# Optimization experiments

Hardware: AMD Instinct MI355X
Metric: run time of the kernel (lower is better)

The kernel has to match this reference:

```python
import jax, jax.numpy as jnp
import numpy as np

D_MODEL, D_STATE, D_CONV, D_INNER, DT_RANK = 1024, 16, 4, 2048, 64
B_SZ, L = 4, 2048

def setup_inputs() -> dict:
    key = jax.random.key(0)
    ks = jax.random.split(key, 7)
    return {
        "hidden_states": jax.random.normal(ks[0], (B_SZ, L, D_MODEL), jnp.float32),
        "in_proj_w": jax.random.normal(ks[1], (2 * D_INNER, D_MODEL), jnp.float32) * (D_MODEL ** -0.5),
        "conv_w": jax.random.normal(ks[2], (D_INNER, 1, D_CONV), jnp.float32) * 0.5,
        "conv_b": jax.random.normal(ks[3], (D_INNER,), jnp.float32) * 0.1,
        "x_proj_w": jax.random.normal(ks[4], (DT_RANK + 2 * D_STATE, D_INNER), jnp.float32) * (D_INNER ** -0.5),
        "dt_proj_w": jax.random.normal(ks[5], (D_INNER, DT_RANK), jnp.float32) * (DT_RANK ** -0.5),
        "A_log": jax.random.uniform(ks[6], (D_INNER, D_STATE), jnp.float32, 0.0, 2.0),
    }

def reference(hidden_states, in_proj_w, conv_w, conv_b, x_proj_w, dt_proj_w, A_log):
    b, l, d = hidden_states.shape
    # in_proj: (b,l,d) x (2*d_inner,d)^T -> (b, 2*d_inner, l)
    xz = jnp.einsum('bld,ed->bel', hidden_states, in_proj_w)
    x, z = jnp.split(xz, 2, axis=1)  # each (b, d_inner, l); z unused downstream
    A = -jnp.exp(A_log)              # (d_inner, d_state)
    # causal depthwise conv1d (left pad d_conv-1) + SiLU
    x = jax.lax.conv_general_dilated(
        x, conv_w, window_strides=(1,), padding=[(D_CONV - 1, 0)],
        feature_group_count=D_INNER,
        dimension_numbers=('NCH', 'OIH', 'NCH'))
    x = jax.nn.silu(x + conv_b[None, :, None])  # (b, d_inner, l)
    # x_proj: (b,l,dt_rank+2*d_state)
    x_dbl = jnp.einsum('bdl,ed->ble', x, x_proj_w)
    dt, B_mat, C_mat = jnp.split(x_dbl, [DT_RANK, DT_RANK + D_STATE], axis=-1)
    dt = jnp.einsum('blr,dr->bdl', dt, dt_proj_w)          # (b, d_inner, l), no bias
    B_mat = jnp.swapaxes(B_mat, 1, 2)                      # (b, d_state, l)
    C_mat = jnp.swapaxes(C_mat, 1, 2)                      # (b, d_state, l)
    return (dt, A, B_mat, C_mat, x)
```

## Files before the change

### kernel.cpp

```cpp
#include <hip/hip_runtime.h>
#include <hip/hip_bf16.h>
#include <math.h>

#define D_MODEL 1024
#define D_STATE 16
#define D_CONV  4
#define D_INNER 2048
#define DT_RANK 64
#define B_SZ    4
#define L_SEQ   2048

#define OFF_DT 0
#define OFF_A  (B_SZ * D_INNER * L_SEQ)
#define OFF_B  (OFF_A + D_INNER * D_STATE)
#define OFF_C  (OFF_B + B_SZ * D_STATE * L_SEQ)
#define OFF_X  (OFF_C + B_SZ * D_STATE * L_SEQ)

typedef __attribute__((ext_vector_type(8))) short bf16x8;
typedef __attribute__((ext_vector_type(8))) unsigned short us8;
typedef __attribute__((ext_vector_type(4))) float f32x4;
typedef unsigned short ushort_t;
typedef unsigned int uint_t;

static __device__ __forceinline__ ushort_t f2bf(float f) {
  __hip_bfloat16 h = __float2bfloat16(f);
  return *(ushort_t*)&h;
}
static __device__ __forceinline__ float bf2f(ushort_t u) {
  union { uint_t u; float f; } c;
  c.u = ((uint_t)u) << 16;
  return c.f;
}

#define N4_HS   (B_SZ * L_SEQ * D_MODEL / 4)
#define N4_W    (D_INNER * D_MODEL / 4)
#define N4_XW   ((DT_RANK + 2 * D_STATE) * D_INNER / 4)
#define N4_DW   (D_INNER * DT_RANK / 4)
#define N4_Z0   (B_SZ * DT_RANK * L_SEQ / 4)
#define N4_Z1   (2 * B_SZ * D_STATE * L_SEQ / 4)
#define N4_A    (D_INNER * D_STATE / 4)
#define N4_TOT  (N4_HS + N4_W + N4_XW + N4_DW + N4_Z0 + N4_Z1 + N4_A)

__global__ __launch_bounds__(256) void k_prep(
    const float4* __restrict__ hs, const float4* __restrict__ ipw,
    const float4* __restrict__ xpw, const float4* __restrict__ dpw,
    const float4* __restrict__ alog,
    ushort4* __restrict__ bfHS, ushort4* __restrict__ bfW,
    ushort4* __restrict__ xwb, ushort4* __restrict__ dwb,
    float4* __restrict__ z0, float4* __restrict__ z1,
    float4* __restrict__ aout) {
  int i = blockIdx.x * 256 + threadIdx.x;
  if (i < N4_HS) {
    float4 v = hs[i];
    ushort4 o; o.x = f2bf(v.x); o.y = f2bf(v.y); o.z = f2bf(v.z); o.w = f2bf(v.w);
    bfHS[i] = o;
    return;
  }
  i -= N4_HS;
  if (i < N4_W) {
    float4 v = ipw[i];
    ushort4 o; o.x = f2bf(v.x); o.y = f2bf(v.y); o.z = f2bf(v.z); o.w = f2bf(v.w);
    bfW[i] = o;
    return;
  }
  i -= N4_W;
  if (i < N4_XW) {
    float4 v = xpw[i];
    ushort4 o; o.x = f2bf(v.x); o.y = f2bf(v.y); o.z = f2bf(v.z); o.w = f2bf(v.w);
    xwb[i] = o;
    return;
  }
  i -= N4_XW;
  if (i < N4_DW) {
    float4 v = dpw[i];
    ushort4 o; o.x = f2bf(v.x); o.y = f2bf(v.y); o.z = f2bf(v.z); o.w = f2bf(v.w);
    dwb[i] = o;
    return;
  }
  i -= N4_DW;
  if (i < N4_Z0) { z0[i] = (float4){0.f, 0.f, 0.f, 0.f}; return; }
  i -= N4_Z0;
  if (i < N4_Z1) { z1[i] = (float4){0.f, 0.f, 0.f, 0.f}; return; }
  i -= N4_Z1;
  if (i < N4_A) {
    float4 v = alog[i];
    float4 o;
    o.x = -expf(v.x); o.y = -expf(v.y); o.z = -expf(v.z); o.w = -expf(v.w);
    aout[i] = o;
  }
}

__global__ __launch_bounds__(256) void k_inproj_mfma(
    const ushort_t* __restrict__ Wb,
    const ushort_t* __restrict__ HSb,
    ushort_t* __restrict__ Cout) {
  const int flat = blockIdx.x + 16 * blockIdx.y + 256 * blockIdx.z;
  const int swz  = (flat & 7) * 128 + (flat >> 3);
  const int bn = swz & 15;
  const int bm = (swz >> 4) & 15;
  const int b  = swz >> 8;

  __shared__ ushort_t sh[128 * 136];
  const int tid  = threadIdx.x;
  const int wv   = tid >> 6;
  const int lane = tid & 63;
  const int wr = wv >> 1, wc = wv & 1;

  const int srow = tid >> 2;
  const int ss   = tid & 3;

  const ushort_t* Ag = Wb + (size_t)(bm * 128) * D_MODEL;
  const ushort_t* Bg = HSb + (size_t)b * L_SEQ * D_MODEL
                           + (size_t)(bn * 128) * D_MODEL;

  f32x4 acc[4][4];
#pragma unroll
  for (int i = 0; i < 4; ++i)
#pragma unroll
    for (int j = 0; j < 4; ++j) acc[i][j] = (f32x4){0.f, 0.f, 0.f, 0.f};

  const int ksel = lane >> 4;
  const int frow = lane & 15;

#define STAGE_IN(BUF, K0)                                                        \
  do {                                                                           \
    _Pragma("unroll")                                                            \
    for (int q = 0; q < 2; ++q) {                                                \
      int row = q * 64 + srow;                                                   \
      int xs  = ss ^ ((row >> 1) & 3);                                           \
      const ushort_t* ga = Ag + (size_t)row * D_MODEL + (K0) + xs * 8;           \
      const ushort_t* gb = Bg + (size_t)row * D_MODEL + (K0) + xs * 8;           \
      ushort_t* la = sh + (BUF) * 8192 + (q * 256 + wv * 64) * 8;                \
      ushort_t* lb = sh + (BUF) * 8192 + 4096 + (q * 256 + wv * 64) * 8;         \
      __builtin_amdgcn_global_load_lds((const __attribute__((address_space(1))) void*)ga, \
                                       (__attribute__((address_space(3))) void*)la, 16, 0, 0); \
      __builtin_amdgcn_global_load_lds((const __attribute__((address_space(1))) void*)gb, \
                                       (__attribute__((address_space(3))) void*)lb, 16, 0, 0); \
    }                                                                            \
  } while (0)

#define COMPUTE(BUF)                                                             \
  do {                                                                           \
    const ushort_t* Ab = sh + (BUF) * 8192;                                      \
    const ushort_t* Bb = sh + (BUF) * 8192 + 4096;                               \
    bf16x8 af[4], bfr[4];                                                        \
    _Pragma("unroll")                                                            \
    for (int m = 0; m < 4; ++m) {                                                \
      int row = wr * 64 + m * 16 + frow;                                         \
      af[m] = *(const bf16x8*)(Ab + (row * 4 + (ksel ^ ((row >> 1) & 3))) * 8);  \
    }                                                                            \
    _Pragma("unroll")                                                            \
    for (int n = 0; n < 4; ++n) {                                                \
      int row = wc * 64 + n * 16 + frow;                                         \
      bfr[n] = *(const bf16x8*)(Bb + (row * 4 + (ksel ^ ((row >> 1) & 3))) * 8); \
    }                                                                            \
    _Pragma("unroll")                                                            \
    for (int m = 0; m < 4; ++m)                                                  \
      _Pragma("unroll")                                                          \
      for (int n = 0; n < 4; ++n)                                                \
        acc[m][n] = __builtin_amdgcn_mfma_f32_16x16x32_bf16(af[m], bfr[n], acc[m][n], 0, 0, 0); \
  } while (0)

  STAGE_IN(0, 0);
  STAGE_IN(1, 32);
  asm volatile("s_waitcnt vmcnt(4)" ::: "memory");
  __builtin_amdgcn_s_barrier();

  for (int t = 0; t < 30; ++t) {
    COMPUTE(t & 1);
    __builtin_amdgcn_sched_barrier(0);
    __builtin_amdgcn_s_barrier();
    STAGE_IN(t & 1, (t + 2) * 32);
    asm volatile("s_waitcnt vmcnt(4)" ::: "memory");
    __builtin_amdgcn_s_barrier();
    __builtin_amdgcn_sched_barrier(0);
  }
  COMPUTE(0);
  __builtin_amdgcn_sched_barrier(0);
  __builtin_amdgcn_s_barrier();
  asm volatile("s_waitcnt vmcnt(0)" ::: "memory");
  __builtin_amdgcn_s_barrier();
  COMPUTE(1);
#undef STAGE_IN
#undef COMPUTE

  __syncthreads();

  const int crow0 = (lane >> 4) * 4;
  const int ccol  = lane & 15;
#pragma unroll
  for (int m = 0; m < 4; ++m) {
#pragma unroll
    for (int n = 0; n < 4; ++n) {
      int r0 = wr * 64 + m * 16 + crow0;
      int c  = wc * 64 + n * 16 + ccol;
#pragma unroll
      for (int i = 0; i < 4; ++i)
        sh[(r0 + i) * 136 + c] = f2bf(acc[m][n][i]);
    }
  }
  __syncthreads();
  ushort_t* Cb = Cout + (size_t)b * D_INNER * L_SEQ
                      + (size_t)(bm * 128) * L_SEQ + bn * 128;
#pragma unroll
  for (int q = 0; q < 8; ++q) {
    int idx = q * 256 + tid;
    int r   = idx >> 4;
    int c16 = idx & 15;
    us8 v = *(const us8*)(sh + r * 136 + c16 * 8);
    *(us8*)(Cb + (size_t)r * L_SEQ + c16 * 8) = v;
  }
}

__global__ __launch_bounds__(256) void k_xproj_fused(
    const ushort_t* __restrict__ XWb,
    const ushort_t* __restrict__ Xpre,
    const float* __restrict__ CW,
    const float* __restrict__ CB,
    float* __restrict__ Xout,
    float* __restrict__ XDBL,
    float* __restrict__ OutB,
    float* __restrict__ OutC) {
  const int ln = blockIdx.x;
  const int sk = blockIdx.y;
  const int b  = blockIdx.z;
  __shared__ ushort_t As[96 * 40];
  __shared__ ushort_t Bs[64 * 34];
  const int tid  = threadIdx.x;
  const int wv   = tid >> 6;
  const int lane = tid & 63;
  const int wr = wv >> 1, wc = wv & 1;
  const int ksel = lane >> 4;
  const int frow = lane & 15;

  f32x4 acc[3][2];
#pragma unroll
  for (int i = 0; i < 3; ++i)
#pragma unroll
    for (int j = 0; j < 2; ++j) acc[i][j] = (f32x4){0.f, 0.f, 0.f, 0.f};

  for (int k0 = 0; k0 < 512; k0 += 32) {
    const int koff = sk * 512 + k0;
    {
      int row = tid >> 2, s = tid & 3;
      bf16x8 v = *(const bf16x8*)(XWb + (size_t)row * D_INNER + koff + s * 8);
      *(bf16x8*)(As + row * 40 + s * 8) = v;
      if (tid < 128) {
        int row2 = 64 + (tid >> 2);
        bf16x8 v2 = *(const bf16x8*)(XWb + (size_t)row2 * D_INNER + koff + s * 8);
        *(bf16x8*)(As + row2 * 40 + s * 8) = v2;
      }
    }
    {
      int n4 = tid & 15;
      int kp = tid >> 4;
      int l0 = ln * 64 + 4 * n4;
      float sv[2][4];
#pragma unroll
      for (int r = 0; r < 2; ++r) {
        int d = koff + 2 * kp + r;
        const ushort_t* row = Xpre + ((size_t)b * D_INNER + d) * L_SEQ;
        ushort4 cur = *(const ushort4*)(row + l0);
        float em3 = 0.f, em2 = 0.f, em1 = 0.f;
        if (l0 >= 4) {
          ushort4 pv = *(const ushort4*)(row + l0 - 4);
          em3 = bf2f(pv.y); em2 = bf2f(pv.z); em1 = bf2f(pv.w);
        }
        float ee[7] = {em3, em2, em1, bf2f(cur.x), bf2f(cur.y), bf2f(cur.z), bf2f(cur.w)};
        float4 w = *(const float4*)(CW + d * 4);
        float bias = CB[d];
#pragma unroll
        for (int i = 0; i < 4; ++i) {
          float v = w.x * ee[i] + w.y * ee[i + 1] + w.z * ee[i + 2] + w.w * ee[i + 3] + bias;
          sv[r][i] = v / (1.f + expf(-v));
        }
        *(float4*)(Xout + ((size_t)b * D_INNER + d) * L_SEQ + l0) =
            make_float4(sv[r][0], sv[r][1], sv[r][2], sv[r][3]);
      }
#pragma unroll
      for (int i = 0; i < 4; ++i) {
        uint_t pk = (uint_t)f2bf(sv[0][i]) | ((uint_t)f2bf(sv[1][i]) << 16);
        *(uint_t*)(Bs + (4 * n4 + i) * 34 + 2 * kp) = pk;
      }
    }
    __syncthreads();

    bf16x8 af[3], bfr[2];
#pragma unroll
    for (int mi = 0; mi < 3; ++mi) {
      int row = wr * 48 + mi * 16 + frow;
      af[mi] = *(const bf16x8*)(As + row * 40 + ksel * 8);
    }
#pragma unroll
    for (int ni = 0; ni < 2; ++ni) {
      int n = wc * 32 + ni * 16 + frow;
      const uint_t* p = (const uint_t*)(Bs + n * 34);
      union { uint_t u[4]; bf16x8 v; } fr;
#pragma unroll
      for (int q = 0; q < 4; ++q) fr.u[q] = p[ksel * 4 + q];
      bfr[ni] = fr.v;
    }
#pragma unroll
    for (int mi = 0; mi < 3; ++mi)
#pragma unroll
      for (int ni = 0; ni < 2; ++ni)
        acc[mi][ni] = __builtin_amdgcn_mfma_f32_16x16x32_bf16(af[mi], bfr[ni], acc[mi][ni], 0, 0, 0);
    __syncthreads();
  }

  const int crow0 = (lane >> 4) * 4;
  const int ccol  = lane & 15;
#pragma unroll
  for (int mi = 0; mi < 3; ++mi) {
    int e0 = wr * 48 + mi * 16 + crow0;
    float* base;
    int eoff;
    if (e0 < 64)      { base = XDBL + (size_t)b * 64 * L_SEQ; eoff = e0; }
    else if (e0 < 80) { base = OutB + (size_t)b * D_STATE * L_SEQ; eoff = e0 - 64; }
    else              { base = OutC + (size_t)b * D_STATE * L_SEQ; eoff = e0 - 80; }
#pragma unroll
    for (int ni = 0; ni < 2; ++ni) {
      int l = ln * 64 + wc * 32 + ni * 16 + ccol;
#pragma unroll
      for (int r = 0; r < 4; ++r)
        atomicAdd(base + (size_t)(eoff + r) * L_SEQ + l, acc[mi][ni][r]);
    }
  }
}

__global__ __launch_bounds__(256) void k_dt_mfma(
    const ushort_t* __restrict__ DWb,
    const float* __restrict__ XDBL,
    float* __restrict__ DT) {
  const int ln = blockIdx.x;
  const int dm = blockIdx.y;
  const int b  = blockIdx.z;
  __shared__ ushort_t As[128 * 72];
  __shared__ ushort_t Bs[128 * 68];
  const int tid  = threadIdx.x;
  const int wv   = tid >> 6;
  const int lane = tid & 63;
  const int wr = wv >> 1, wc = wv & 1;
  const int ksel = lane >> 4;
  const int frow = lane & 15;

#pragma unroll
  for (int q = 0; q < 4; ++q) {
    int u = tid + 256 * q;
    int row = u >> 3, s = u & 7;
    *(bf16x8*)(As + row * 72 + s * 8) =
        *(const bf16x8*)(DWb + (size_t)(dm * 128 + row) * DT_RANK + s * 8);
  }
#pragma unroll
  for (int q = 0; q < 4; ++q) {
    int u = tid + 256 * q;
    int n4 = u & 31;
    int kp = u >> 5;
    const float* g = XDBL + ((size_t)b * DT_RANK + 2 * kp) * L_SEQ + ln * 128 + 4 * n4;
    float4 x0 = *(const float4*)g;
    float4 x1 = *(const float4*)(g + L_SEQ);
    float e0[4] = {x0.x, x0.y, x0.z, x0.w};
    float e1[4] = {x1.x, x1.y, x1.z, x1.w};
#pragma unroll
    for (int i = 0; i < 4; ++i) {
      uint_t pk = (uint_t)f2bf(e0[i]) | ((uint_t)f2bf(e1[i]) << 16);
      *(uint_t*)(Bs + (4 * n4 + i) * 68 + 2 * kp) = pk;
    }
  }
  __syncthreads();

  f32x4 acc[4][4];
#pragma unroll
  for (int i = 0; i < 4; ++i)
#pragma unroll
    for (int j = 0; j < 4; ++j) acc[i][j] = (f32x4){0.f, 0.f, 0.f, 0.f};

#pragma unroll
  for (int ks = 0; ks < 2; ++ks) {
    bf16x8 af[4], bfr[4];
#pragma unroll
    for (int m = 0; m < 4; ++m) {
      int row = wr * 64 + m * 16 + frow;
      af[m] = *(const bf16x8*)(As + row * 72 + ks * 32 + ksel * 8);
    }
#pragma unroll
    for (int n = 0; n < 4; ++n) {
      int nn = wc * 64 + n * 16 + frow;
      bfr[n] = *(const bf16x8*)(Bs + nn * 68 + ks * 32 + ksel * 8);
    }
#pragma unroll
    for (int m = 0; m < 4; ++m)
#pragma unroll
      for (int n = 0; n < 4; ++n)
        acc[m][n] = __builtin_amdgcn_mfma_f32_16x16x32_bf16(af[m], bfr[n], acc[m][n], 0, 0, 0);
  }

  const int crow0 = (lane >> 4) * 4;
  const int ccol  = lane & 15;
  float* Cb = DT + (size_t)b * D_INNER * L_SEQ;
#pragma unroll
  for (int m = 0; m < 4; ++m) {
    int gr0 = dm * 128 + wr * 64 + m * 16 + crow0;
#pragma unroll
    for (int n = 0; n < 4; ++n) {
      int gc = ln * 128 + wc * 64 + n * 16 + ccol;
#pragma unroll
      for (int i = 0; i < 4; ++i)
        Cb[(size_t)(gr0 + i) * L_SEQ + gc] = acc[m][n][i];
    }
  }
}

extern "C" void kernel_launch(void* const* d_in, const int* in_sizes, int n_in,
                              void* d_out, int out_size, void* d_ws, size_t ws_size,
                              hipStream_t stream) {
  const float* hs   = (const float*)d_in[0];
  const float* ipw  = (const float*)d_in[1];
  const float* cw   = (const float*)d_in[2];
  const float* cb   = (const float*)d_in[3];
  const float* xpw  = (const float*)d_in[4];
  const float* dpw  = (const float*)d_in[5];
  const float* alog = (const float*)d_in[6];

  float* out    = (float*)d_out;
  float* dt_out = out + OFF_DT;
  float* a_out  = out + OFF_A;
  float* b_out  = out + OFF_B;
  float* c_out  = out + OFF_C;
  float* x_out  = out + OFF_X;

  unsigned short* bfHS = (unsigned short*)x_out;
  unsigned short* bfW  = bfHS + (size_t)B_SZ * L_SEQ * D_MODEL;
  unsigned short* xpre = (unsigned short*)dt_out;
  float* xdbl = (float*)d_ws;
  unsigned short* xwb = (unsigned short*)((char*)d_ws + 2097152);
  unsigned short* dwb = (unsigned short*)((char*)d_ws + 2097152 + 393216);

  k_prep<<<dim3((N4_TOT + 255) / 256), 256, 0, stream>>>(
      (const float4*)hs, (const float4*)ipw, (const float4*)xpw,
      (const float4*)dpw, (const float4*)alog,
      (ushort4*)bfHS, (ushort4*)bfW, (ushort4*)xwb, (ushort4*)dwb,
      (float4*)xdbl, (float4*)b_out, (float4*)a_out);

  k_inproj_mfma<<<dim3(16, 16, 4), 256, 0, stream>>>(bfW, bfHS, xpre);
  k_xproj_fused<<<dim3(32, 4, 4), 256, 0, stream>>>(xwb, xpre, cw, cb,
                                                    x_out, xdbl, b_out, c_out);
  k_dt_mfma<<<dim3(16, 16, 4), 256, 0, stream>>>(dwb, xdbl, dt_out);
}
```

Baseline: 125.3 us.

## Enlarge in-proj GEMM tile to 256x256 with 8 waves and K64 stages

The in-projection MFMA GEMM goes from 128x128 tiles with K=32 stages on 256 threads to 256x256 tiles with K=64 stages on 512 threads. Each wave now computes a 128x64 sub-tile, and raised s_setprio wraps the MFMA bursts. The larger tile raises arithmetic intensity, cuts global and LDS traffic per FLOP, and halves the number of barrier-separated k-steps. The costs are 128KB of LDS per block, which means one block per CU, 128 accumulator registers per thread, only 256 blocks in the grid, and an epilogue written in two passes.

```diff
diff --git a/kernel.cpp b/kernel.cpp
--- a/kernel.cpp
+++ b/kernel.cpp
@@ -90,88 +90,97 @@
   }
 }
 
-__global__ __launch_bounds__(256) void k_inproj_mfma(
+__global__ __launch_bounds__(512, 2) void k_inproj_mfma(
     const ushort_t* __restrict__ Wb,
     const ushort_t* __restrict__ HSb,
     ushort_t* __restrict__ Cout) {
-  const int flat = blockIdx.x + 16 * blockIdx.y + 256 * blockIdx.z;
-  const int swz  = (flat & 7) * 128 + (flat >> 3);
-  const int bn = swz & 15;
-  const int bm = (swz >> 4) & 15;
-  const int b  = swz >> 8;
-
-  __shared__ ushort_t sh[128 * 136];
+  const int flat = blockIdx.x + 8 * blockIdx.y + 64 * blockIdx.z;
+  const int swz  = (flat & 7) * 32 + (flat >> 3);
+  const int bn = swz & 7;
+  const int bm = (swz >> 3) & 7;
+  const int b  = swz >> 6;
+
+  __shared__ ushort_t sh[65536];
   const int tid  = threadIdx.x;
-  const int wv   = tid >> 6;
+  const int w    = tid >> 6;
   const int lane = tid & 63;
-  const int wr = wv >> 1, wc = wv & 1;
-
-  const int srow = tid >> 2;
-  const int ss   = tid & 3;
-
-  const ushort_t* Ag = Wb + (size_t)(bm * 128) * D_MODEL;
-  const ushort_t* Bg = HSb + (size_t)b * L_SEQ * D_MODEL
-                           + (size_t)(bn * 128) * D_MODEL;
-
-  f32x4 acc[4][4];
-#pragma unroll
-  for (int i = 0; i < 4; ++i)
-#pragma unroll
-    for (int j = 0; j < 4; ++j) acc[i][j] = (f32x4){0.f, 0.f, 0.f, 0.f};
-
+  const int wm = w >> 2, wn = w & 3;
   const int ksel = lane >> 4;
   const int frow = lane & 15;
-
-#define STAGE_IN(BUF, K0)                                                        \
+  const int sr = tid >> 2;
+  const int ss = tid & 3;
+
+  const ushort_t* Ag = Wb + (size_t)(bm * 256) * D_MODEL;
+  const ushort_t* Bg = HSb + (size_t)b * L_SEQ * D_MODEL
+                           + (size_t)(bn * 256) * D_MODEL;
+
+  f32x4 acc[8][4];
+#pragma unroll
+  for (int m = 0; m < 8; ++m)
+#pragma unroll
+    for (int n = 0; n < 4; ++n) acc[m][n] = (f32x4){0.f, 0.f, 0.f, 0.f};
+
+  const int sxs = ss ^ ((sr >> 1) & 3);
+
+#define STAGE(BUF, T)                                                            \
   do {                                                                           \
     _Pragma("unroll")                                                            \
-    for (int q = 0; q < 2; ++q) {                                                \
-      int row = q * 64 + srow;                                                   \
-      int xs  = ss ^ ((row >> 1) & 3);                                           \
-      const ushort_t* ga = Ag + (size_t)row * D_MODEL + (K0) + xs * 8;           \
-      const ushort_t* gb = Bg + (size_t)row * D_MODEL + (K0) + xs * 8;           \
-      ushort_t* la = sh + (BUF) * 8192 + (q * 256 + wv * 64) * 8;                \
-      ushort_t* lb = sh + (BUF) * 8192 + 4096 + (q * 256 + wv * 64) * 8;         \
-      __builtin_amdgcn_global_load_lds((const __attribute__((address_space(1))) void*)ga, \
-                                       (__attribute__((address_space(3))) void*)la, 16, 0, 0); \
-      __builtin_amdgcn_global_load_lds((const __attribute__((address_space(1))) void*)gb, \
-                                       (__attribute__((address_space(3))) void*)lb, 16, 0, 0); \
+    for (int mh = 0; mh < 4; ++mh) {                                             \
+      const ushort_t* gbase = (mh < 2) ? Ag : Bg;                                \
+      const ushort_t* grow = gbase + (size_t)((mh & 1) * 128 + sr) * D_MODEL     \
+                                   + (T) * 64 + sxs * 8;                         \
+      _Pragma("unroll")                                                          \
+      for (int q = 0; q < 2; ++q) {                                              \
+        ushort_t* dst = sh + (BUF) * 32768 + (mh >> 1) * 16384                   \
+                           + (mh & 1) * 8192 + q * 4096 + tid * 8;               \
+        __builtin_amdgcn_global_load_lds(                                        \
+            (const __attribute__((address_space(1))) void*)(grow + q * 32),      \
+            (__attribute__((address_space(3))) void*)dst, 16, 0, 0);             \
+      }                                                                          \
     }                                                                            \
   } while (0)
 
 #define COMPUTE(BUF)                                                             \
   do {                                                                           \
-    const ushort_t* Ab = sh + (BUF) * 8192;                                      \
-    const ushort_t* Bb = sh + (BUF) * 8192 + 4096;                               \
-    bf16x8 af[4], bfr[4];                                                        \
     _Pragma("unroll")                                                            \
-    for (int m = 0; m < 4; ++m) {                                                \
-      int row = wr * 64 + m * 16 + frow;                                         \
-      af[m] = *(const bf16x8*)(Ab + (row * 4 + (ksel ^ ((row >> 1) & 3))) * 8);  \
+    for (int ks = 0; ks < 2; ++ks) {                                             \
+      bf16x8 af[8], bfr[4];                                                      \
+      _Pragma("unroll")                                                          \
+      for (int m = 0; m < 8; ++m) {                                              \
+        int r = m * 16 + frow;                                                   \
+        af[m] = *(const bf16x8*)(sh + (BUF) * 32768 + wm * 8192 + ks * 4096      \
+                                 + (r * 4 + (ksel ^ ((r >> 1) & 3))) * 8);       \
+      }                                                                          \
+      _Pragma("unroll")                                                          \
+      for (int n = 0; n < 4; ++n) {                                              \
+        int ll = wn * 64 + n * 16 + frow;                                        \
+        int h = ll >> 7, r = ll & 127;                                           \
+        bfr[n] = *(const bf16x8*)(sh + (BUF) * 32768 + 16384 + h * 8192          \
+                                  + ks * 4096                                    \
+                                  + (r * 4 + (ksel ^ ((r >> 1) & 3))) * 8);      \
+      }                                                                          \
+      __builtin_amdgcn_s_setprio(1);                                             \
+      _Pragma("unroll")                                                          \
+      for (int m = 0; m < 8; ++m)                                                \
+        _Pragma("unroll")                                                        \
+        for (int n = 0; n < 4; ++n)                                              \
+          acc[m][n] = __builtin_amdgcn_mfma_f32_16x16x32_bf16(af[m], bfr[n],     \
+                                                              acc[m][n], 0, 0, 0); \
+      __builtin_amdgcn_s_setprio(0);                                             \
     }                                                                            \
-    _Pragma("unroll")                                                            \
-    for (int n = 0; n < 4; ++n) {                                                \
-      int row = wc * 64 + n * 16 + frow;                                         \
-      bfr[n] = *(const bf16x8*)(Bb + (row * 4 + (ksel ^ ((row >> 1) & 3))) * 8); \
-    }                                                                            \
-    _Pragma("unroll")                                                            \
-    for (int m = 0; m < 4; ++m)                                                  \
-      _Pragma("unroll")                                                          \
-      for (int n = 0; n < 4; ++n)                                                \
-        acc[m][n] = __builtin_amdgcn_mfma_f32_16x16x32_bf16(af[m], bfr[n], acc[m][n], 0, 0, 0); \
   } while (0)
 
-  STAGE_IN(0, 0);
-  STAGE_IN(1, 32);
-  asm volatile("s_waitcnt vmcnt(4)" ::: "memory");
+  STAGE(0, 0);
+  STAGE(1, 1);
+  asm volatile("s_waitcnt vmcnt(8)" ::: "memory");
   __builtin_amdgcn_s_barrier();
 
-  for (int t = 0; t < 30; ++t) {
+  for (int t = 0; t < 14; ++t) {
     COMPUTE(t & 1);
     __builtin_amdgcn_sched_barrier(0);
     __builtin_amdgcn_s_barrier();
-    STAGE_IN(t & 1, (t + 2) * 32);
-    asm volatile("s_waitcnt vmcnt(4)" ::: "memory");
+    STAGE(t & 1, t + 2);
+    asm volatile("s_waitcnt vmcnt(8)" ::: "memory");
     __builtin_amdgcn_s_barrier();
     __builtin_amdgcn_sched_barrier(0);
   }
@@ -181,34 +190,38 @@
   asm volatile("s_waitcnt vmcnt(0)" ::: "memory");
   __builtin_amdgcn_s_barrier();
   COMPUTE(1);
-#undef STAGE_IN
+#undef STAGE
 #undef COMPUTE
 
   __syncthreads();
 
   const int crow0 = (lane >> 4) * 4;
   const int ccol  = lane & 15;
-#pragma unroll
-  for (int m = 0; m < 4; ++m) {
-#pragma unroll
-    for (int n = 0; n < 4; ++n) {
-      int r0 = wr * 64 + m * 16 + crow0;
-      int c  = wc * 64 + n * 16 + ccol;
-#pragma unroll
-      for (int i = 0; i < 4; ++i)
-        sh[(r0 + i) * 136 + c] = f2bf(acc[m][n][i]);
-    }
-  }
-  __syncthreads();
-  ushort_t* Cb = Cout + (size_t)b * D_INNER * L_SEQ
-                      + (size_t)(bm * 128) * L_SEQ + bn * 128;
-#pragma unroll
-  for (int q = 0; q < 8; ++q) {
-    int idx = q * 256 + tid;
-    int r   = idx >> 4;
-    int c16 = idx & 15;
-    us8 v = *(const us8*)(sh + r * 136 + c16 * 8);
-    *(us8*)(Cb + (size_t)r * L_SEQ + c16 * 8) = v;
+  ushort_t* Cb = Cout + (size_t)b * D_INNER * L_SEQ;
+#pragma unroll
+  for (int p = 0; p < 2; ++p) {
+    if (wm == p) {
+#pragma unroll
+      for (int m = 0; m < 8; ++m)
+#pragma unroll
+        for (int n = 0; n < 4; ++n) {
+          int r0 = m * 16 + crow0;
+          int c  = wn * 64 + n * 16 + ccol;
+#pragma unroll
+          for (int i = 0; i < 4; ++i)
+            sh[(r0 + i) * 272 + c] = f2bf(acc[m][n][i]);
+        }
+    }
+    __syncthreads();
+#pragma unroll
+    for (int q = 0; q < 8; ++q) {
+      int idx = q * 512 + tid;
+      int r   = idx >> 5;
+      int c8  = idx & 31;
+      us8 v = *(const us8*)(sh + r * 272 + c8 * 8);
+      *(us8*)(Cb + (size_t)(bm * 256 + p * 128 + r) * L_SEQ + bn * 256 + c8 * 8) = v;
+    }
+    __syncthreads();
   }
 }
 
@@ -442,7 +455,7 @@
       (ushort4*)bfHS, (ushort4*)bfW, (ushort4*)xwb, (ushort4*)dwb,
       (float4*)xdbl, (float4*)b_out, (float4*)a_out);
 
-  k_inproj_mfma<<<dim3(16, 16, 4), 256, 0, stream>>>(bfW, bfHS, xpre);
+  k_inproj_mfma<<<dim3(8, 8, 4), 512, 0, stream>>>(bfW, bfHS, xpre);
   k_xproj_fused<<<dim3(32, 4, 4), 256, 0, stream>>>(xwb, xpre, cw, cb,
                                                     x_out, xdbl, b_out, c_out);
   k_dt_mfma<<<dim3(16, 16, 4), 256, 0, stream>>>(dwb, xdbl, dt_out);
```

Measured after the change: 119.8 us, median of 2. 4.4% less time.
